# Kernel tuning notes

Measured on AMD Instinct MI355X. Metric: run time of the kernel, lower is better.

## Reference

```python
import jax, jax.numpy as jnp
import numpy as np

NUM_CLASSES = 21
BATCH = 128
ANCHORS = 8732


def setup_inputs() -> dict:
    key = jax.random.key(0)
    k1, k2, k3, k4 = jax.random.split(key, 4)
    loc_preds = jax.random.normal(k1, (BATCH, ANCHORS, 4), dtype=jnp.float32)
    loc_targets = jax.random.normal(k2, (BATCH, ANCHORS, 4), dtype=jnp.float32)
    cls_preds = jax.random.normal(k3, (BATCH, ANCHORS, NUM_CLASSES), dtype=jnp.float32)
    cls_targets = jax.random.randint(k4, (BATCH, ANCHORS), 0, NUM_CLASSES, dtype=jnp.int64)
    return {
        "loc_preds": loc_preds,
        "loc_targets": loc_targets,
        "cls_preds": cls_preds,
        "cls_targets": cls_targets,
    }


def _ssd_loss(loc_preds, loc_targets, cls_preds, cls_targets):
    pos = cls_targets > 0                                   # [B, A] bool
    num_pos = pos.sum().astype(loc_preds.dtype)

    # masked smooth-L1 (beta = 1.0), sum reduction over positive anchors
    diff = jnp.abs(loc_preds - loc_targets)                 # [B, A, 4]
    sl1 = jnp.where(diff < 1.0, 0.5 * diff * diff, diff - 0.5)
    loc_loss = jnp.sum(sl1 * pos[..., None].astype(sl1.dtype))

    # per-anchor cross entropy
    logp = jax.nn.log_softmax(cls_preds, axis=-1)           # [B, A, C]
    tgt = jnp.clip(cls_targets, 0, NUM_CLASSES - 1)
    ce = -jnp.take_along_axis(logp, tgt[..., None], axis=-1)[..., 0]  # [B, A]
    ce = jnp.where(cls_targets < 0, 0.0, ce)

    # hard negative mining via double argsort (rank of each anchor's loss)
    mined = ce * (pos.astype(ce.dtype) - 1.0)               # 0 at pos, -loss at neg
    idx = jnp.argsort(mined, axis=1)
    rank = jnp.argsort(idx, axis=1)
    num_pos_per = pos.sum(axis=1, keepdims=True)            # [B, 1]
    neg = rank < 3 * num_pos_per                            # [B, A]

    cls_loss = jnp.sum(jnp.where(pos | neg, ce, 0.0))
    return (loc_loss + cls_loss) / num_pos


def reference(loc_preds, loc_targets, cls_preds, cls_targets):
    return _ssd_loss(loc_preds, loc_targets, cls_preds, cls_targets)
```

## Files before the change

### kernel.cpp

```cpp
#include <hip/hip_runtime.h>
#include <stdint.h>

namespace {

constexpr int B    = 128;
constexpr int A    = 8732;
constexpr int NC   = 21;
constexpr int TILE = 128;
constexpr int T    = 128;
constexpr int TPR  = (A + TILE - 1) / TILE;
constexpr int CH   = 16;
constexpr int NBLK = B * CH;
constexpr int THREADS = 256;

__device__ __forceinline__ float waveReduceSum(float v) {
#pragma unroll
    for (int off = 32; off; off >>= 1) v += __shfl_xor(v, off, 64);
    return v;
}
__device__ __forceinline__ int waveReduceSumI(int v) {
#pragma unroll
    for (int off = 32; off; off >>= 1) v += __shfl_xor(v, off, 64);
    return v;
}

__global__ __launch_bounds__(T) void main_kernel(
    const float* __restrict__ locp,
    const float* __restrict__ loct,
    const float* __restrict__ clsp,
    const int*   __restrict__ tgt,
    float* __restrict__ locPart,
    float* __restrict__ clsPart,
    int*   __restrict__ posPart)
{
    const int b   = blockIdx.y;
    const int c   = blockIdx.x;
    const int tid = threadIdx.x;
    const long rowBase = (long)b * A;

    __shared__ __align__(16) float scls[TILE * NC];
    float4* const scls4 = (float4*)scls;

    float accLoc = 0.f, accCe = 0.f;
    int accPos = 0;

    float4 r0, r1, r2, r3, r4, r5, lpN, ltN;
    int tN = 0, nN = 0, nf4N = 0;

    auto issue = [&](int tile) {
        const int a0 = tile * TILE;
        nN   = (A - a0 < TILE) ? (A - a0) : TILE;
        nf4N = nN * NC / 4;
        const float4* __restrict__ src = (const float4*)(clsp + (rowBase + a0) * NC);
        r0 = src[tid];
        if (tid + 1 * T < nf4N) r1 = src[tid + 1 * T];
        if (tid + 2 * T < nf4N) r2 = src[tid + 2 * T];
        if (tid + 3 * T < nf4N) r3 = src[tid + 3 * T];
        if (tid + 4 * T < nf4N) r4 = src[tid + 4 * T];
        if (tid + 5 * T < nf4N) r5 = src[tid + 5 * T];
        if (tid < nN) {
            const long i = rowBase + a0 + tid;
            tN  = tgt[i];
            lpN = *(const float4*)(locp + i * 4);
            ltN = *(const float4*)(loct + i * 4);
        } else tN = 0;
    };
    auto writeLds = [&](int nf4) {
        scls4[tid] = r0;
        if (tid + 1 * T < nf4) scls4[tid + 1 * T] = r1;
        if (tid + 2 * T < nf4) scls4[tid + 2 * T] = r2;
        if (tid + 3 * T < nf4) scls4[tid + 3 * T] = r3;
        if (tid + 4 * T < nf4) scls4[tid + 4 * T] = r4;
        if (tid + 5 * T < nf4) scls4[tid + 5 * T] = r5;
    };

    int tile = c;
    issue(tile);
    writeLds(nf4N);
    __syncthreads();
    float4 lp = lpN, lt = ltN;
    int tt = tN, n = nN;

    for (;;) {
        const int nxt = tile + CH;
        const bool hasNext = nxt < TPR;
        if (hasNext) issue(nxt);

        if (tid < n) {
            const float* __restrict__ x = scls + tid * NC;
            float xs[NC];
#pragma unroll
            for (int cc = 0; cc < NC; ++cc) xs[cc] = x[cc];
            float m = xs[0];
#pragma unroll
            for (int cc = 1; cc < NC; ++cc) m = fmaxf(m, xs[cc]);
            float s = 0.f;
#pragma unroll
            for (int cc = 0; cc < NC; ++cc) s += __expf(xs[cc] - m);
            const int tc = tt < 0 ? 0 : (tt > NC - 1 ? NC - 1 : tt);
            accCe += (tt < 0) ? 0.f : (m + __logf(s) - xs[tc]);
            if (tt > 0) {
                ++accPos;
                float d;
                d = fabsf(lp.x - lt.x); accLoc += (d < 1.f) ? 0.5f * d * d : d - 0.5f;
                d = fabsf(lp.y - lt.y); accLoc += (d < 1.f) ? 0.5f * d * d : d - 0.5f;
                d = fabsf(lp.z - lt.z); accLoc += (d < 1.f) ? 0.5f * d * d : d - 0.5f;
                d = fabsf(lp.w - lt.w); accLoc += (d < 1.f) ? 0.5f * d * d : d - 0.5f;
            }
        }
        if (!hasNext) break;

        __syncthreads();
        writeLds(nf4N);
        __syncthreads();
        lp = lpN; lt = ltN; tt = tN; n = nN;
        tile = nxt;
    }

    __shared__ float sLoc[2], sCls[2];
    __shared__ int sPos[2];
    const int wid = tid >> 6, lane = tid & 63;
    float wl = waveReduceSum(accLoc);
    float wc = waveReduceSum(accCe);
    int   wp = waveReduceSumI(accPos);
    if (lane == 0) { sLoc[wid] = wl; sCls[wid] = wc; sPos[wid] = wp; }
    __syncthreads();
    if (tid == 0) {
        const int blk = b * CH + c;
        locPart[blk] = sLoc[0] + sLoc[1];
        clsPart[blk] = sCls[0] + sCls[1];
        posPart[blk] = sPos[0] + sPos[1];
    }
}

__global__ __launch_bounds__(THREADS) void mining_kernel(
    const float* __restrict__ clsp,
    const int*   __restrict__ tgt,
    const int*   __restrict__ posPart,
    float* __restrict__ corr)
{
    const int b = blockIdx.x;
    const int wid = threadIdx.x >> 6, lane = threadIdx.x & 63;

    int cnt = (threadIdx.x < CH) ? posPart[b * CH + threadIdx.x] : 0;
    __shared__ int sCnt[4];
    int wcnt = waveReduceSumI(cnt);
    if (lane == 0) sCnt[wid] = wcnt;
    __syncthreads();
    const int K = 3 * (sCnt[0] + sCnt[1] + sCnt[2] + sCnt[3]);

    float corrv = 0.f;
    if (K < A) {
        __shared__ float mined[A];
        for (int i = threadIdx.x; i < A; i += THREADS) {
            const long idx = (long)b * A + i;
            const int t = tgt[idx];
            float ce = 0.f;
            if (t >= 0) {
                const float* __restrict__ x = clsp + idx * (long)NC;
                float m = x[0];
                for (int cc = 1; cc < NC; ++cc) m = fmaxf(m, x[cc]);
                float s = 0.f;
                for (int cc = 0; cc < NC; ++cc) s += __expf(x[cc] - m);
                const int tc = t > NC - 1 ? NC - 1 : t;
                ce = m + __logf(s) - x[tc];
            }
            mined[i] = (t > 0) ? 0.f : -ce;
        }
        __syncthreads();

        float c0 = 0.f;
        for (int i = threadIdx.x; i < A; i += THREADS) {
            const int t = tgt[(long)b * A + i];
            if (t > 0) continue;
            const float mi = mined[i];
            int rank = 0;
            for (int j = 0; j < A; ++j) {
                const float mj = mined[j];
                rank += (mj < mi || (mj == mi && j < i)) ? 1 : 0;
            }
            if (rank >= K) c0 += mi;
        }
        __shared__ float sC[4];
        float wcorr = waveReduceSum(c0);
        if (lane == 0) sC[wid] = wcorr;
        __syncthreads();
        corrv = sC[0] + sC[1] + sC[2] + sC[3];
    }
    if (threadIdx.x == 0) corr[b] = corrv;
}

__global__ __launch_bounds__(THREADS) void finalize_kernel(
    const float* __restrict__ locPart,
    const float* __restrict__ clsPart,
    const int*   __restrict__ posPart,
    const float* __restrict__ corr,
    float* __restrict__ out)
{
    float L = 0.f, C = 0.f;
    int P = 0;
    for (int i = threadIdx.x; i < NBLK; i += THREADS) {
        L += locPart[i];
        C += clsPart[i];
        P += posPart[i];
    }
    if (threadIdx.x < B) C += corr[threadIdx.x];

    __shared__ float sL[4], sC[4];
    __shared__ int sP[4];
    const int wid = threadIdx.x >> 6, lane = threadIdx.x & 63;
    float wl = waveReduceSum(L);
    float wc = waveReduceSum(C);
    int   wp = waveReduceSumI(P);
    if (lane == 0) { sL[wid] = wl; sC[wid] = wc; sP[wid] = wp; }
    __syncthreads();
    if (threadIdx.x == 0) {
        const float loc = sL[0] + sL[1] + sL[2] + sL[3];
        const float cls = sC[0] + sC[1] + sC[2] + sC[3];
        const int   np  = sP[0] + sP[1] + sP[2] + sP[3];
        out[0] = (loc + cls) / (float)np;
    }
}

}

extern "C" void kernel_launch(void* const* d_in, const int* in_sizes, int n_in,
                              void* d_out, int out_size, void* d_ws, size_t ws_size,
                              hipStream_t stream) {
    const float* locp = (const float*)d_in[0];
    const float* loct = (const float*)d_in[1];
    const float* clsp = (const float*)d_in[2];
    const int*   tgt  = (const int*)d_in[3];

    float* locPart = (float*)d_ws;
    float* clsPart = locPart + NBLK;
    int*   posPart = (int*)(clsPart + NBLK);
    float* corr    = (float*)(posPart + NBLK);
    float* out     = (float*)d_out;

    hipLaunchKernelGGL(main_kernel, dim3(CH, B), dim3(T), 0, stream,
                       locp, loct, clsp, tgt, locPart, clsPart, posPart);
    hipLaunchKernelGGL(mining_kernel, dim3(B), dim3(THREADS), 0, stream,
                       clsp, tgt, posPart, corr);
    hipLaunchKernelGGL(finalize_kernel, dim3(1), dim3(THREADS), 0, stream,
                       locPart, clsPart, posPart, corr, out);
}
```

Baseline: 183.6 us.

## Replace LDS-staged tiling with direct per-anchor float4 loads over contiguous spans

The main kernel no longer stages class logits through shared memory with double-buffered tiles and barriers. Each thread now handles one anchor at a time. It loads the six aligned float4 words that cover that anchor's 21 logits and masks out the extra lanes. Each block walks one contiguous span of anchors with 256 threads. The softmax also drops the max subtraction, and location data is loaded only for positive anchors. This removes barrier and LDS traffic but reads overlapping, less coalesced memory, and the log-sum-exp can overflow for large logits.

Result: faster. 179.3 us (-2.3%).

```diff
diff --git a/kernel.cpp b/kernel.cpp
--- a/kernel.cpp
+++ b/kernel.cpp
@@ -6,10 +6,9 @@
 constexpr int B    = 128;
 constexpr int A    = 8732;
 constexpr int NC   = 21;
-constexpr int TILE = 128;
-constexpr int T    = 128;
-constexpr int TPR  = (A + TILE - 1) / TILE;
 constexpr int CH   = 16;
+constexpr int SPAN = (A + CH - 1) / CH;
+constexpr int T    = 256;
 constexpr int NBLK = B * CH;
 constexpr int THREADS = 256;
 
@@ -33,92 +32,61 @@
     float* __restrict__ clsPart,
     int*   __restrict__ posPart)
 {
-    const int b   = blockIdx.y;
-    const int c   = blockIdx.x;
-    const int tid = threadIdx.x;
+    const int b     = blockIdx.y;
+    const int c     = blockIdx.x;
+    const int tid   = threadIdx.x;
+    const int start = c * SPAN;
+    const int end   = (start + SPAN < A) ? (start + SPAN) : A;
     const long rowBase = (long)b * A;
-
-    __shared__ __align__(16) float scls[TILE * NC];
-    float4* const scls4 = (float4*)scls;
 
     float accLoc = 0.f, accCe = 0.f;
     int accPos = 0;
 
-    float4 r0, r1, r2, r3, r4, r5, lpN, ltN;
-    int tN = 0, nN = 0, nf4N = 0;
-
-    auto issue = [&](int tile) {
-        const int a0 = tile * TILE;
-        nN   = (A - a0 < TILE) ? (A - a0) : TILE;
-        nf4N = nN * NC / 4;
-        const float4* __restrict__ src = (const float4*)(clsp + (rowBase + a0) * NC);
-        r0 = src[tid];
-        if (tid + 1 * T < nf4N) r1 = src[tid + 1 * T];
-        if (tid + 2 * T < nf4N) r2 = src[tid + 2 * T];
-        if (tid + 3 * T < nf4N) r3 = src[tid + 3 * T];
-        if (tid + 4 * T < nf4N) r4 = src[tid + 4 * T];
-        if (tid + 5 * T < nf4N) r5 = src[tid + 5 * T];
-        if (tid < nN) {
-            const long i = rowBase + a0 + tid;
-            tN  = tgt[i];
-            lpN = *(const float4*)(locp + i * 4);
-            ltN = *(const float4*)(loct + i * 4);
-        } else tN = 0;
-    };
-    auto writeLds = [&](int nf4) {
-        scls4[tid] = r0;
-        if (tid + 1 * T < nf4) scls4[tid + 1 * T] = r1;
-        if (tid + 2 * T < nf4) scls4[tid + 2 * T] = r2;
-        if (tid + 3 * T < nf4) scls4[tid + 3 * T] = r3;
-        if (tid + 4 * T < nf4) scls4[tid + 4 * T] = r4;
-        if (tid + 5 * T < nf4) scls4[tid + 5 * T] = r5;
-    };
-
-    int tile = c;
-    issue(tile);
-    writeLds(nf4N);
-    __syncthreads();
-    float4 lp = lpN, lt = ltN;
-    int tt = tN, n = nN;
-
-    for (;;) {
-        const int nxt = tile + CH;
-        const bool hasNext = nxt < TPR;
-        if (hasNext) issue(nxt);
-
-        if (tid < n) {
-            const float* __restrict__ x = scls + tid * NC;
-            float xs[NC];
+    for (int a = start + tid; a < end; a += T) {
+        const long ga = rowBase + a;
+        const int  t  = tgt[ga];
+        const long f0 = ga * NC;
+        const float4* __restrict__ w = (const float4*)clsp + (f0 >> 2);
+        const int off = (int)(f0 & 3);
+
+        float4 q0 = w[0], q1 = w[1], q2 = w[2], q3 = w[3], q4 = w[4], q5 = w[5];
+
+        float4 lp, lt;
+        if (t > 0) {
+            lp = *(const float4*)(locp + ga * 4);
+            lt = *(const float4*)(loct + ga * 4);
+        }
+        const int tc = t < 0 ? 0 : (t > NC - 1 ? NC - 1 : t);
+        const float xt = clsp[f0 + tc];
+
+        float v[24];
+        v[0]=q0.x; v[1]=q0.y; v[2]=q0.z; v[3]=q0.w;
+        v[4]=q1.x; v[5]=q1.y; v[6]=q1.z; v[7]=q1.w;
+        v[8]=q2.x; v[9]=q2.y; v[10]=q2.z; v[11]=q2.w;
+        v[12]=q3.x; v[13]=q3.y; v[14]=q3.z; v[15]=q3.w;
+        v[16]=q4.x; v[17]=q4.y; v[18]=q4.z; v[19]=q4.w;
+        v[20]=q5.x; v[21]=q5.y; v[22]=q5.z; v[23]=q5.w;
+
+        float s = 0.f;
 #pragma unroll
-            for (int cc = 0; cc < NC; ++cc) xs[cc] = x[cc];
-            float m = xs[0];
-#pragma unroll
-            for (int cc = 1; cc < NC; ++cc) m = fmaxf(m, xs[cc]);
-            float s = 0.f;
-#pragma unroll
-            for (int cc = 0; cc < NC; ++cc) s += __expf(xs[cc] - m);
-            const int tc = tt < 0 ? 0 : (tt > NC - 1 ? NC - 1 : tt);
-            accCe += (tt < 0) ? 0.f : (m + __logf(s) - xs[tc]);
-            if (tt > 0) {
-                ++accPos;
-                float d;
-                d = fabsf(lp.x - lt.x); accLoc += (d < 1.f) ? 0.5f * d * d : d - 0.5f;
-                d = fabsf(lp.y - lt.y); accLoc += (d < 1.f) ? 0.5f * d * d : d - 0.5f;
-                d = fabsf(lp.z - lt.z); accLoc += (d < 1.f) ? 0.5f * d * d : d - 0.5f;
-                d = fabsf(lp.w - lt.w); accLoc += (d < 1.f) ? 0.5f * d * d : d - 0.5f;
-            }
-        }
-        if (!hasNext) break;
-
-        __syncthreads();
-        writeLds(nf4N);
-        __syncthreads();
-        lp = lpN; lt = ltN; tt = tN; n = nN;
-        tile = nxt;
-    }
-
-    __shared__ float sLoc[2], sCls[2];
-    __shared__ int sPos[2];
+        for (int j = 0; j < 24; ++j) {
+            const float e = __expf(v[j]);
+            s += (j >= off && j < off + NC) ? e : 0.f;
+        }
+        accCe += (t < 0) ? 0.f : (__logf(s) - xt);
+
+        if (t > 0) {
+            ++accPos;
+            float d;
+            d = fabsf(lp.x - lt.x); accLoc += (d < 1.f) ? 0.5f * d * d : d - 0.5f;
+            d = fabsf(lp.y - lt.y); accLoc += (d < 1.f) ? 0.5f * d * d : d - 0.5f;
+            d = fabsf(lp.z - lt.z); accLoc += (d < 1.f) ? 0.5f * d * d : d - 0.5f;
+            d = fabsf(lp.w - lt.w); accLoc += (d < 1.f) ? 0.5f * d * d : d - 0.5f;
+        }
+    }
+
+    __shared__ float sLoc[4], sCls[4];
+    __shared__ int sPos[4];
     const int wid = tid >> 6, lane = tid & 63;
     float wl = waveReduceSum(accLoc);
     float wc = waveReduceSum(accCe);
@@ -127,9 +95,9 @@
     __syncthreads();
     if (tid == 0) {
         const int blk = b * CH + c;
-        locPart[blk] = sLoc[0] + sLoc[1];
-        clsPart[blk] = sCls[0] + sCls[1];
-        posPart[blk] = sPos[0] + sPos[1];
+        locPart[blk] = sLoc[0] + sLoc[1] + sLoc[2] + sLoc[3];
+        clsPart[blk] = sCls[0] + sCls[1] + sCls[2] + sCls[3];
+        posPart[blk] = sPos[0] + sPos[1] + sPos[2] + sPos[3];
     }
 }
 
```
